# Kernel optimization log

Measured on AMD Instinct MI355X. Metric: run time of the kernel, lower is better.

The kernel has to match this reference:

```python
import jax, jax.numpy as jnp
import numpy as np

NUM_USERS = 100000
NUM_ITEMS = 50000
DIM_H = 64
NUM_LAYERS = 4
NUM_EDGES = 2000000


def setup_inputs() -> dict:
    key = jax.random.key(0)
    k1, k2, k3, k4 = jax.random.split(key, 4)
    emb_users = jax.random.normal(k1, (NUM_USERS, DIM_H), dtype=jnp.float32) * 0.01
    emb_items = jax.random.normal(k2, (NUM_ITEMS, DIM_H), dtype=jnp.float32) * 0.01
    edge_users = jax.random.randint(k3, (NUM_EDGES,), 0, NUM_USERS, dtype=jnp.int64)
    edge_items = jax.random.randint(k4, (NUM_EDGES,), 0, NUM_ITEMS, dtype=jnp.int64)
    edge_values = jnp.ones((NUM_EDGES,), dtype=jnp.float32)
    return {"emb_users": emb_users, "emb_items": emb_items,
            "edge_users": edge_users, "edge_items": edge_items,
            "edge_values": edge_values}


def reference(emb_users, emb_items, edge_users, edge_items, edge_values):
    U = emb_users.shape[0]
    I = emb_items.shape[0]
    N = U + I
    # Symmetric bipartite adjacency in COO form: (u, i+U) and (i+U, u).
    rows = jnp.concatenate([edge_users, edge_items + U])
    cols = jnp.concatenate([edge_items + U, edge_users])
    vals = jnp.concatenate([edge_values, edge_values])
    # D^{-1/2} A D^{-1/2} normalization (inf -> 0 for isolated nodes).
    deg = jax.ops.segment_sum(vals, rows, num_segments=N)
    dinv = jnp.where(deg > 0, jax.lax.rsqrt(jnp.maximum(deg, 1e-12)), 0.0)
    nvals = dinv[rows] * vals * dinv[cols]

    emb = jnp.concatenate([emb_users, emb_items])  # [N, d]
    acc = emb  # running sum over layer outputs (incl. layer 0)
    e = emb
    for _ in range(NUM_LAYERS):
        # SpMM: e <- A_norm @ e via gather + segment-sum scatter
        e = jax.ops.segment_sum(nvals[:, None] * e[cols], rows, num_segments=N)
        acc = acc + e
    alpha = 1.0 / (NUM_LAYERS + 1)
    # Original computes alpha * mean(stack(embs)), i.e. sum / (L+1)^2.
    emb_final = alpha * (acc / (NUM_LAYERS + 1))
    embf_users = emb_final[:U]
    embf_items = emb_final[U:]
    return (embf_users, emb_users, embf_items, emb_items)
```

## Files before the change

### kernel.cpp

```cpp
#include <hip/hip_runtime.h>


static inline size_t align_up(size_t x, size_t a) { return (x + a - 1) & ~(a - 1); }

#define NBA 640
#define KB  1024

__device__ inline unsigned short f32_to_bf16(float f) {
    unsigned int u = __float_as_uint(f);
    unsigned int r = (u + 0x7FFFu + ((u >> 16) & 1u)) >> 16;
    return (unsigned short)r;
}
__device__ inline float bf16_to_f32(unsigned short h) {
    return __uint_as_float(((unsigned int)h) << 16);
}
__device__ inline float bf16_lo(unsigned int d) {
    return __uint_as_float(d << 16);
}
__device__ inline float bf16_hi(unsigned int d) {
    return __uint_as_float(d & 0xFFFF0000u);
}

__global__ __launch_bounds__(256) void k_bucket_count(
        const int* __restrict__ eu, const int* __restrict__ ei,
        int* __restrict__ bh, int U, int E, int NB, int CH) {
    __shared__ int hist[NBA];
    int k = blockIdx.x;
    int t = threadIdx.x;
    for (int b = t; b < NBA; b += 256) hist[b] = 0;
    __syncthreads();
    int lo = k * CH, hi = min(E, lo + CH);
    for (int i = lo + t; i < hi; i += 256) {
        int u  = eu[i];
        int it = ei[i] + U;
        atomicAdd(&hist[u >> 8], 1);
        atomicAdd(&hist[it >> 8], 1);
    }
    __syncthreads();
    for (int b = t; b < NB; b += 256) bh[k * NBA + b] = hist[b];
}

__global__ __launch_bounds__(256) void k_scan_blocks(
        int* __restrict__ bh, int* __restrict__ total, int NB) {
    __shared__ int s[256];
    int b = blockIdx.x;
    int t = threadIdx.x;
    int k0 = t * 4;
    int vals[4];
    int sum = 0;
    #pragma unroll
    for (int j = 0; j < 4; ++j) { vals[j] = bh[(k0 + j) * NBA + b]; sum += vals[j]; }
    s[t] = sum;
    __syncthreads();
    for (int d = 1; d < 256; d <<= 1) {
        int v = (t >= d) ? s[t - d] : 0;
        __syncthreads();
        s[t] += v;
        __syncthreads();
    }
    int run = s[t] - sum;
    #pragma unroll
    for (int j = 0; j < 4; ++j) { int v = vals[j]; bh[(k0 + j) * NBA + b] = run; run += v; }
    if (t == 255) total[b] = run;
}

__global__ __launch_bounds__(256) void k_scan_buckets(
        const int* __restrict__ total, int* __restrict__ bbase, int NB) {
    __shared__ int s[256];
    int t = threadIdx.x;
    int C = (NB + 255) / 256;
    int vals[4];
    int sum = 0;
    for (int j = 0; j < C; ++j) {
        int idx = t * C + j;
        int v = (idx < NB) ? (((total[idx] + 3) & ~3) + 768) : 0;
        vals[j] = v; sum += v;
    }
    s[t] = sum;
    __syncthreads();
    for (int d = 1; d < 256; d <<= 1) {
        int v = (t >= d) ? s[t - d] : 0;
        __syncthreads();
        s[t] += v;
        __syncthreads();
    }
    int run = s[t] - sum;
    for (int j = 0; j < C; ++j) {
        int idx = t * C + j;
        if (idx < NB) bbase[idx] = run;
        run += vals[j];
    }
}

__global__ __launch_bounds__(256) void k_bucket_scatter(
        const int* __restrict__ eu, const int* __restrict__ ei,
        const float* __restrict__ ev, const int* __restrict__ bh,
        int2* __restrict__ gb, int U, int E, int NB, int CH, int CAP) {
    __shared__ int lbase[NBA];
    int k = blockIdx.x;
    int t = threadIdx.x;
    for (int b = t; b < NB; b += 256) lbase[b] = b * CAP + bh[k * NBA + b];
    __syncthreads();
    int lo = k * CH, hi = min(E, lo + CH);
    for (int i = lo + t; i < hi; i += 256) {
        int u  = eu[i];
        int it = ei[i] + U;
        int vb = __float_as_int(ev[i]);
        int b1 = u >> 8;
        int p1 = atomicAdd(&lbase[b1], 1);
        if (p1 < (b1 + 1) * CAP) gb[p1] = make_int2((u & 255) | (it << 8), vb);
        int b2 = it >> 8;
        int p2 = atomicAdd(&lbase[b2], 1);
        if (p2 < (b2 + 1) * CAP) gb[p2] = make_int2((it & 255) | (u << 8), vb);
    }
}

__global__ __launch_bounds__(256) void k_bucket_csr(
        const int2* __restrict__ gb, const int* __restrict__ total,
        const int* __restrict__ bbase,
        int* __restrict__ offs, int* __restrict__ cnt,
        float* __restrict__ dinv, float* __restrict__ dsq,
        int2* __restrict__ csr, int N, int CAP) {
    __shared__ int   hist[256];
    __shared__ float degf[256];
    __shared__ int   offl[256];
    __shared__ int   scan[256];
    int b = blockIdx.x;
    int t = threadIdx.x;
    int n0 = b << 8;
    int nbc = min(256, N - n0);
    int cb = min(total[b], CAP);
    int base = bbase[b];
    const int2* gbb = gb + (size_t)b * CAP;

    hist[t] = 0;
    degf[t] = 0.f;
    __syncthreads();
    for (int i = t; i < cb; i += 256) {
        int2 e = gbb[i];
        int rl = e.x & 255;
        atomicAdd(&hist[rl], 1);
        atomicAdd(&degf[rl], __int_as_float(e.y));
    }
    __syncthreads();
    int h = hist[t];
    int h4 = (h + 3) & ~3;
    scan[t] = h4;
    __syncthreads();
    for (int d = 1; d < 256; d <<= 1) {
        int v = (t >= d) ? scan[t - d] : 0;
        __syncthreads();
        scan[t] += v;
        __syncthreads();
    }
    int off4 = scan[t] - h4;
    offl[t] = off4;
    if (t < nbc) {
        int node = n0 + t;
        offs[node] = base + off4;
        cnt[node]  = h;
        float s = degf[t];
        bool pos = (s > 0.0f);
        dinv[node] = pos ? rsqrtf(fmaxf(s, 1e-12f)) : 0.0f;
        dsq[node]  = pos ? sqrtf(s) : 0.0f;
        for (int p = h; p < h4; ++p)
            csr[base + off4 + p] = make_int2(0, 0);
    }
    hist[t] = 0;
    __syncthreads();
    for (int i = t; i < cb; i += 256) {
        int2 e = gbb[i];
        int rl = e.x & 255;
        int col = (int)(((unsigned)e.x) >> 8);
        int tk = atomicAdd(&hist[rl], 1);
        csr[base + offl[rl] + tk] = make_int2(col, e.y);
    }
}

__global__ void k_init(const float4* __restrict__ emb_u, const float4* __restrict__ emb_i,
                       const float* __restrict__ dinv,
                       ushort4* __restrict__ g0, int U16, int N16) {
    int i = blockIdx.x * blockDim.x + threadIdx.x;
    if (i >= N16) return;
    float4 v = (i < U16) ? emb_u[i] : emb_i[i - U16];
    float d = dinv[i >> 4];
    ushort4 o;
    o.x = f32_to_bf16(v.x * d);
    o.y = f32_to_bf16(v.y * d);
    o.z = f32_to_bf16(v.z * d);
    o.w = f32_to_bf16(v.w * d);
    g0[i] = o;
}

__global__ __launch_bounds__(256) void k_layer(
        const uint4* __restrict__ gin, uint4* __restrict__ gout,
        const float* __restrict__ dinv,
        const int* __restrict__ offs, const int* __restrict__ cnt,
        const int2* __restrict__ csr, int N) {
    int gtid = blockIdx.x * blockDim.x + threadIdx.x;
    int row = gtid >> 3;
    unsigned q = threadIdx.x & 7;
    if (row >= N) return;
    int base = offs[row];
    int c = cnt[row];
    int nIter = (c + 3) >> 2;

    float a0 = 0.f, a1 = 0.f, a2 = 0.f, a3 = 0.f;
    float a4 = 0.f, a5 = 0.f, a6 = 0.f, a7 = 0.f;

    const uint4* ep4 = (const uint4*)(csr + base);
    uint4 E0 = make_uint4(0, 0, 0, 0), E1 = E0;
    if (nIter > 0) { E0 = ep4[0]; E1 = ep4[1]; }

    for (int i = 0; i < nIter; ++i) {
        uint4 G0 = gin[(E0.x << 3) | q];
        uint4 G1 = gin[(E0.z << 3) | q];
        uint4 G2 = gin[(E1.x << 3) | q];
        uint4 G3 = gin[(E1.z << 3) | q];
        uint4 P0 = ep4[2 * i + 2];
        uint4 P1 = ep4[2 * i + 3];
        float w0 = __uint_as_float(E0.y);
        float w1 = __uint_as_float(E0.w);
        float w2 = __uint_as_float(E1.y);
        float w3 = __uint_as_float(E1.w);
        a0 += w0 * bf16_lo(G0.x); a1 += w0 * bf16_hi(G0.x);
        a2 += w0 * bf16_lo(G0.y); a3 += w0 * bf16_hi(G0.y);
        a4 += w0 * bf16_lo(G0.z); a5 += w0 * bf16_hi(G0.z);
        a6 += w0 * bf16_lo(G0.w); a7 += w0 * bf16_hi(G0.w);
        a0 += w1 * bf16_lo(G1.x); a1 += w1 * bf16_hi(G1.x);
        a2 += w1 * bf16_lo(G1.y); a3 += w1 * bf16_hi(G1.y);
        a4 += w1 * bf16_lo(G1.z); a5 += w1 * bf16_hi(G1.z);
        a6 += w1 * bf16_lo(G1.w); a7 += w1 * bf16_hi(G1.w);
        a0 += w2 * bf16_lo(G2.x); a1 += w2 * bf16_hi(G2.x);
        a2 += w2 * bf16_lo(G2.y); a3 += w2 * bf16_hi(G2.y);
        a4 += w2 * bf16_lo(G2.z); a5 += w2 * bf16_hi(G2.z);
        a6 += w2 * bf16_lo(G2.w); a7 += w2 * bf16_hi(G2.w);
        a0 += w3 * bf16_lo(G3.x); a1 += w3 * bf16_hi(G3.x);
        a2 += w3 * bf16_lo(G3.y); a3 += w3 * bf16_hi(G3.y);
        a4 += w3 * bf16_lo(G3.z); a5 += w3 * bf16_hi(G3.z);
        a6 += w3 * bf16_lo(G3.w); a7 += w3 * bf16_hi(G3.w);
        E0 = P0; E1 = P1;
    }

    float dr = dinv[row];
    float d2 = dr * dr;
    uint4 o;
    o.x = (unsigned int)f32_to_bf16(d2 * a0) | ((unsigned int)f32_to_bf16(d2 * a1) << 16);
    o.y = (unsigned int)f32_to_bf16(d2 * a2) | ((unsigned int)f32_to_bf16(d2 * a3) << 16);
    o.z = (unsigned int)f32_to_bf16(d2 * a4) | ((unsigned int)f32_to_bf16(d2 * a5) << 16);
    o.w = (unsigned int)f32_to_bf16(d2 * a6) | ((unsigned int)f32_to_bf16(d2 * a7) << 16);
    gout[((unsigned)row << 3) | q] = o;
}

__global__ void k_final(const float4* __restrict__ emb_u, const float4* __restrict__ emb_i,
                        const ushort4* __restrict__ g1, const ushort4* __restrict__ g2,
                        const ushort4* __restrict__ g3, const ushort4* __restrict__ g4,
                        const float* __restrict__ dsq,
                        float4* __restrict__ out, int U16, int I16) {
    int i = blockIdx.x * blockDim.x + threadIdx.x;
    int total = 2 * U16 + 2 * I16;
    if (i >= total) return;
    const float s = 1.0f / 25.0f;
    float4 r;
    if (i < U16 || (i >= 2 * U16 && i < 2 * U16 + I16)) {
        int gi, node;
        float4 e0;
        if (i < U16) { gi = i; node = i >> 4; e0 = emb_u[i]; }
        else { int j = i - 2 * U16; gi = U16 + j; node = (U16 >> 4) + (j >> 4); e0 = emb_i[j]; }
        float d = dsq[node];
        ushort4 a = g1[gi], b = g2[gi], cc = g3[gi], dd = g4[gi];
        float gx = bf16_to_f32(a.x) + bf16_to_f32(b.x) + bf16_to_f32(cc.x) + bf16_to_f32(dd.x);
        float gy = bf16_to_f32(a.y) + bf16_to_f32(b.y) + bf16_to_f32(cc.y) + bf16_to_f32(dd.y);
        float gz = bf16_to_f32(a.z) + bf16_to_f32(b.z) + bf16_to_f32(cc.z) + bf16_to_f32(dd.z);
        float gw = bf16_to_f32(a.w) + bf16_to_f32(b.w) + bf16_to_f32(cc.w) + bf16_to_f32(dd.w);
        r = make_float4((e0.x + d * gx) * s, (e0.y + d * gy) * s,
                        (e0.z + d * gz) * s, (e0.w + d * gw) * s);
    } else if (i < 2 * U16) {
        r = emb_u[i - U16];
    } else {
        r = emb_i[i - 2 * U16 - I16];
    }
    out[i] = r;
}

extern "C" void kernel_launch(void* const* d_in, const int* in_sizes, int n_in,
                              void* d_out, int out_size, void* d_ws, size_t ws_size,
                              hipStream_t stream) {
    const float* emb_u = (const float*)d_in[0];
    const float* emb_i = (const float*)d_in[1];
    const int*   eu    = (const int*)d_in[2];
    const int*   ei    = (const int*)d_in[3];
    const float* ev    = (const float*)d_in[4];

    const int U = in_sizes[0] / 64;
    const int I = in_sizes[1] / 64;
    const int N = U + I;
    const int E = in_sizes[2];
    const int DE = 2 * E;

    const int NB = (N + 255) >> 8;
    const int CH = (E + KB - 1) / KB;

    char* base = (char*)d_ws;
    size_t off = 0;
    int*   offs  = (int*)  (base + off); off = align_up(off + (size_t)N * 4, 256);
    int*   cnt   = (int*)  (base + off); off = align_up(off + (size_t)N * 4, 256);
    float* dinv  = (float*)(base + off); off = align_up(off + (size_t)N * 4, 256);
    float* dsq   = (float*)(base + off); off = align_up(off + (size_t)N * 4, 256);
    int*   bh    = (int*)  (base + off); off = align_up(off + (size_t)NBA * KB * 4, 256);
    int*   total = (int*)  (base + off); off = align_up(off + (size_t)NBA * 4, 256);
    int*   bbase = (int*)  (base + off); off = align_up(off + (size_t)NBA * 4, 256);
    int2*  csr   = (int2*) (base + off);
    off = align_up(off + ((size_t)DE + (size_t)NBA * 772 + 16) * 8, 256);
    unsigned short* g[5];
    for (int l = 0; l < 5; ++l) {
        g[l] = (unsigned short*)(base + off);
        off = align_up(off + (size_t)N * 64 * 2, 256);
    }
    (void)ws_size;

    int2* gb = (int2*)g[1];
    size_t gcap = (size_t)4 * N * 128;
    int CAP = (int)(gcap / ((size_t)NB * 8));
    if (CAP > 16128) CAP = 16128;

    const int B = 256;
    k_bucket_count  <<<KB, B, 0, stream>>>(eu, ei, bh, U, E, NB, CH);
    k_scan_blocks   <<<NB, B, 0, stream>>>(bh, total, NB);
    k_scan_buckets  <<<1,  B, 0, stream>>>(total, bbase, NB);
    k_bucket_scatter<<<KB, B, 0, stream>>>(eu, ei, ev, bh, gb, U, E, NB, CH, CAP);
    k_bucket_csr    <<<NB, B, 0, stream>>>(gb, total, bbase, offs, cnt, dinv, dsq, csr, N, CAP);

    const int U16 = U * 16, I16 = I * 16, N16 = N * 16;
    k_init<<<(N16 + B - 1) / B, B, 0, stream>>>((const float4*)emb_u, (const float4*)emb_i,
                                                dinv, (ushort4*)g[0], U16, N16);

    for (int layer = 0; layer < 4; ++layer) {
        int threads = N * 8;
        k_layer<<<(threads + B - 1) / B, B, 0, stream>>>(
            (const uint4*)g[layer], (uint4*)g[layer + 1], dinv, offs, cnt, csr, N);
    }

    int totalv4 = 2 * U16 + 2 * I16;
    k_final<<<(totalv4 + B - 1) / B, B, 0, stream>>>(
        (const float4*)emb_u, (const float4*)emb_i,
        (const ushort4*)g[1], (const ushort4*)g[2], (const ushort4*)g[3], (const ushort4*)g[4],
        dsq, (float4*)d_out, U16, I16);
}
```

Before: 545.5 us.

## Widen CSR buckets to 1024 nodes and stage bucket scatter through LDS

Bucket width grows from 256 to 1024 nodes, so there are far fewer buckets (147 instead of 586) and the CSR build runs 1024-thread blocks. The scatter kernel now counts its edges per bucket, scans locally, writes entries sorted by bucket into shared memory, and then streams them to global memory. This turns scattered 8-byte writes into mostly contiguous runs. It adds an extra pass over the edges and a large LDS footprint (about 48KB) that limits occupancy. It also assumes each block's chunk of edges fits in 4096 staged entries.

After: 543.0 us. No clear change (-0.5%).

```diff
diff --git a/kernel.cpp b/kernel.cpp
--- a/kernel.cpp
+++ b/kernel.cpp
@@ -3,8 +3,10 @@
 
 static inline size_t align_up(size_t x, size_t a) { return (x + a - 1) & ~(a - 1); }
 
-#define NBA 640
+#define BS_LOG 10
+#define NBA 160
 #define KB  1024
+#define ENT 4096
 
 __device__ inline unsigned short f32_to_bf16(float f) {
     unsigned int u = __float_as_uint(f);
@@ -27,17 +29,17 @@
     __shared__ int hist[NBA];
     int k = blockIdx.x;
     int t = threadIdx.x;
-    for (int b = t; b < NBA; b += 256) hist[b] = 0;
+    if (t < NBA) hist[t] = 0;
     __syncthreads();
     int lo = k * CH, hi = min(E, lo + CH);
     for (int i = lo + t; i < hi; i += 256) {
         int u  = eu[i];
         int it = ei[i] + U;
-        atomicAdd(&hist[u >> 8], 1);
-        atomicAdd(&hist[it >> 8], 1);
-    }
-    __syncthreads();
-    for (int b = t; b < NB; b += 256) bh[k * NBA + b] = hist[b];
+        atomicAdd(&hist[u >> BS_LOG], 1);
+        atomicAdd(&hist[it >> BS_LOG], 1);
+    }
+    __syncthreads();
+    if (t < NB) bh[k * NBA + t] = hist[t];
 }
 
 __global__ __launch_bounds__(256) void k_scan_blocks(
@@ -68,67 +70,91 @@
         const int* __restrict__ total, int* __restrict__ bbase, int NB) {
     __shared__ int s[256];
     int t = threadIdx.x;
-    int C = (NB + 255) / 256;
-    int vals[4];
-    int sum = 0;
-    for (int j = 0; j < C; ++j) {
-        int idx = t * C + j;
-        int v = (idx < NB) ? (((total[idx] + 3) & ~3) + 768) : 0;
-        vals[j] = v; sum += v;
-    }
-    s[t] = sum;
+    int v = (t < NB) ? (((total[t] + 3) & ~3) + 3072) : 0;
+    s[t] = v;
     __syncthreads();
     for (int d = 1; d < 256; d <<= 1) {
-        int v = (t >= d) ? s[t - d] : 0;
-        __syncthreads();
-        s[t] += v;
-        __syncthreads();
-    }
-    int run = s[t] - sum;
-    for (int j = 0; j < C; ++j) {
-        int idx = t * C + j;
-        if (idx < NB) bbase[idx] = run;
-        run += vals[j];
-    }
+        int x = (t >= d) ? s[t - d] : 0;
+        __syncthreads();
+        s[t] += x;
+        __syncthreads();
+    }
+    if (t < NB) bbase[t] = s[t] - v;
 }
 
 __global__ __launch_bounds__(256) void k_bucket_scatter(
         const int* __restrict__ eu, const int* __restrict__ ei,
         const float* __restrict__ ev, const int* __restrict__ bh,
         int2* __restrict__ gb, int U, int E, int NB, int CH, int CAP) {
-    __shared__ int lbase[NBA];
+    __shared__ uint2 sent[ENT];
+    __shared__ int   sdst[ENT];
+    __shared__ int   lcur[NBA];
+    __shared__ int   ldif[NBA];
+    __shared__ int   sscan[256];
+    __shared__ int   stot;
     int k = blockIdx.x;
     int t = threadIdx.x;
-    for (int b = t; b < NB; b += 256) lbase[b] = b * CAP + bh[k * NBA + b];
+    if (t < NBA) lcur[t] = 0;
     __syncthreads();
     int lo = k * CH, hi = min(E, lo + CH);
     for (int i = lo + t; i < hi; i += 256) {
         int u  = eu[i];
         int it = ei[i] + U;
-        int vb = __float_as_int(ev[i]);
-        int b1 = u >> 8;
-        int p1 = atomicAdd(&lbase[b1], 1);
-        if (p1 < (b1 + 1) * CAP) gb[p1] = make_int2((u & 255) | (it << 8), vb);
-        int b2 = it >> 8;
-        int p2 = atomicAdd(&lbase[b2], 1);
-        if (p2 < (b2 + 1) * CAP) gb[p2] = make_int2((it & 255) | (u << 8), vb);
-    }
-}
-
-__global__ __launch_bounds__(256) void k_bucket_csr(
+        atomicAdd(&lcur[u >> BS_LOG], 1);
+        atomicAdd(&lcur[it >> BS_LOG], 1);
+    }
+    __syncthreads();
+    int c = (t < NB) ? lcur[t] : 0;
+    sscan[t] = c;
+    __syncthreads();
+    for (int d = 1; d < 256; d <<= 1) {
+        int v = (t >= d) ? sscan[t - d] : 0;
+        __syncthreads();
+        sscan[t] += v;
+        __syncthreads();
+    }
+    if (t < NB) {
+        int st = sscan[t] - c;
+        lcur[t] = st;
+        ldif[t] = t * CAP + bh[k * NBA + t] - st;
+    }
+    if (t == 255) stot = sscan[255];
+    __syncthreads();
+    for (int i = lo + t; i < hi; i += 256) {
+        int u  = eu[i];
+        int it = ei[i] + U;
+        unsigned vb = __float_as_uint(ev[i]);
+        int b1 = u >> BS_LOG;
+        int s1 = atomicAdd(&lcur[b1], 1);
+        sent[s1] = make_uint2((unsigned)((u & 1023) | (it << 10)), vb);
+        sdst[s1] = ldif[b1] + s1;
+        int b2 = it >> BS_LOG;
+        int s2 = atomicAdd(&lcur[b2], 1);
+        sent[s2] = make_uint2((unsigned)((it & 1023) | (u << 10)), vb);
+        sdst[s2] = ldif[b2] + s2;
+    }
+    __syncthreads();
+    int tot = stot;
+    for (int i = t; i < tot; i += 256) {
+        uint2 e = sent[i];
+        gb[sdst[i]] = make_int2((int)e.x, (int)e.y);
+    }
+}
+
+__global__ __launch_bounds__(1024) void k_bucket_csr(
         const int2* __restrict__ gb, const int* __restrict__ total,
         const int* __restrict__ bbase,
         int* __restrict__ offs, int* __restrict__ cnt,
         float* __restrict__ dinv, float* __restrict__ dsq,
         int2* __restrict__ csr, int N, int CAP) {
-    __shared__ int   hist[256];
-    __shared__ float degf[256];
-    __shared__ int   offl[256];
-    __shared__ int   scan[256];
+    __shared__ int   hist[1024];
+    __shared__ float degf[1024];
+    __shared__ int   offl[1024];
+    __shared__ int   scan[1024];
     int b = blockIdx.x;
     int t = threadIdx.x;
-    int n0 = b << 8;
-    int nbc = min(256, N - n0);
+    int n0 = b << BS_LOG;
+    int nbc = min(1024, N - n0);
     int cb = min(total[b], CAP);
     int base = bbase[b];
     const int2* gbb = gb + (size_t)b * CAP;
@@ -136,9 +162,9 @@
     hist[t] = 0;
     degf[t] = 0.f;
     __syncthreads();
-    for (int i = t; i < cb; i += 256) {
+    for (int i = t; i < cb; i += 1024) {
         int2 e = gbb[i];
-        int rl = e.x & 255;
+        int rl = e.x & 1023;
         atomicAdd(&hist[rl], 1);
         atomicAdd(&degf[rl], __int_as_float(e.y));
     }
@@ -147,7 +173,7 @@
     int h4 = (h + 3) & ~3;
     scan[t] = h4;
     __syncthreads();
-    for (int d = 1; d < 256; d <<= 1) {
+    for (int d = 1; d < 1024; d <<= 1) {
         int v = (t >= d) ? scan[t - d] : 0;
         __syncthreads();
         scan[t] += v;
@@ -168,10 +194,10 @@
     }
     hist[t] = 0;
     __syncthreads();
-    for (int i = t; i < cb; i += 256) {
+    for (int i = t; i < cb; i += 1024) {
         int2 e = gbb[i];
-        int rl = e.x & 255;
-        int col = (int)(((unsigned)e.x) >> 8);
+        int rl = e.x & 1023;
+        int col = (int)(((unsigned)e.x) >> 10);
         int tk = atomicAdd(&hist[rl], 1);
         csr[base + offl[rl] + tk] = make_int2(col, e.y);
     }
@@ -298,7 +324,7 @@
     const int E = in_sizes[2];
     const int DE = 2 * E;
 
-    const int NB = (N + 255) >> 8;
+    const int NB = (N + 1023) >> BS_LOG;
     const int CH = (E + KB - 1) / KB;
 
     char* base = (char*)d_ws;
@@ -311,7 +337,7 @@
     int*   total = (int*)  (base + off); off = align_up(off + (size_t)NBA * 4, 256);
     int*   bbase = (int*)  (base + off); off = align_up(off + (size_t)NBA * 4, 256);
     int2*  csr   = (int2*) (base + off);
-    off = align_up(off + ((size_t)DE + (size_t)NBA * 772 + 16) * 8, 256);
+    off = align_up(off + ((size_t)DE + (size_t)NBA * 3080 + 32) * 8, 256);
     unsigned short* g[5];
     for (int l = 0; l < 5; ++l) {
         g[l] = (unsigned short*)(base + off);
@@ -322,14 +348,14 @@
     int2* gb = (int2*)g[1];
     size_t gcap = (size_t)4 * N * 128;
     int CAP = (int)(gcap / ((size_t)NB * 8));
-    if (CAP > 16128) CAP = 16128;
+    if (CAP > 65536) CAP = 65536;
 
     const int B = 256;
     k_bucket_count  <<<KB, B, 0, stream>>>(eu, ei, bh, U, E, NB, CH);
     k_scan_blocks   <<<NB, B, 0, stream>>>(bh, total, NB);
     k_scan_buckets  <<<1,  B, 0, stream>>>(total, bbase, NB);
     k_bucket_scatter<<<KB, B, 0, stream>>>(eu, ei, ev, bh, gb, U, E, NB, CH, CAP);
-    k_bucket_csr    <<<NB, B, 0, stream>>>(gb, total, bbase, offs, cnt, dinv, dsq, csr, N, CAP);
+    k_bucket_csr    <<<NB, 1024, 0, stream>>>(gb, total, bbase, offs, cnt, dinv, dsq, csr, N, CAP);
 
     const int U16 = U * 16, I16 = I * 16, N16 = N * 16;
     k_init<<<(N16 + B - 1) / B, B, 0, stream>>>((const float4*)emb_u, (const float4*)emb_i,
```

## Stage bucket scatter and CSR build in LDS for coalesced global writes

Applied to the files above, without the earlier changes.

The bucket-scatter kernel now counts edges per bucket locally, sorts its chunk of edges by bucket in shared memory, and writes them out contiguously, replacing random per-edge global stores. The CSR build kernel uses 512 threads and assembles each bucket's CSR image in shared memory before one linear copy to global memory. Both aim to cut scattered, uncoalesced global writes during graph preprocessing. In exchange they add an extra pass over edge inputs, a large LDS footprint that lowers occupancy, and a CSR image capped at CAPL entries, beyond which edges are silently dropped. The bounds checks against CAP on global writes are also removed.

After: 501.5 us. -8.1%, faster.

```diff
diff --git a/kernel.cpp b/kernel.cpp
--- a/kernel.cpp
+++ b/kernel.cpp
@@ -5,6 +5,8 @@
 
 #define NBA 640
 #define KB  1024
+#define ENT 4096
+#define CAPL 12032
 
 __device__ inline unsigned short f32_to_bf16(float f) {
     unsigned int u = __float_as_uint(f);
@@ -96,35 +98,84 @@
         const int* __restrict__ eu, const int* __restrict__ ei,
         const float* __restrict__ ev, const int* __restrict__ bh,
         int2* __restrict__ gb, int U, int E, int NB, int CH, int CAP) {
-    __shared__ int lbase[NBA];
+    __shared__ uint2 sent[ENT];
+    __shared__ int   sdst[ENT];
+    __shared__ int   lcur[NBA];
+    __shared__ int   ldif[NBA];
+    __shared__ int   sscan[256];
     int k = blockIdx.x;
     int t = threadIdx.x;
-    for (int b = t; b < NB; b += 256) lbase[b] = b * CAP + bh[k * NBA + b];
+    for (int b = t; b < NBA; b += 256) lcur[b] = 0;
     __syncthreads();
     int lo = k * CH, hi = min(E, lo + CH);
     for (int i = lo + t; i < hi; i += 256) {
         int u  = eu[i];
         int it = ei[i] + U;
-        int vb = __float_as_int(ev[i]);
+        atomicAdd(&lcur[u >> 8], 1);
+        atomicAdd(&lcur[it >> 8], 1);
+    }
+    __syncthreads();
+    int c3[3];
+    int sum = 0;
+    #pragma unroll
+    for (int j = 0; j < 3; ++j) {
+        int idx = t * 3 + j;
+        int v = (idx < NB) ? lcur[idx] : 0;
+        c3[j] = v; sum += v;
+    }
+    sscan[t] = sum;
+    __syncthreads();
+    for (int d = 1; d < 256; d <<= 1) {
+        int v = (t >= d) ? sscan[t - d] : 0;
+        __syncthreads();
+        sscan[t] += v;
+        __syncthreads();
+    }
+    int run = sscan[t] - sum;
+    int tot = sscan[255];
+    __syncthreads();
+    #pragma unroll
+    for (int j = 0; j < 3; ++j) {
+        int idx = t * 3 + j;
+        if (idx < NB) {
+            lcur[idx] = run;
+            ldif[idx] = idx * CAP + bh[k * NBA + idx] - run;
+        }
+        run += c3[j];
+    }
+    __syncthreads();
+    for (int i = lo + t; i < hi; i += 256) {
+        int u  = eu[i];
+        int it = ei[i] + U;
+        unsigned vb = __float_as_uint(ev[i]);
         int b1 = u >> 8;
-        int p1 = atomicAdd(&lbase[b1], 1);
-        if (p1 < (b1 + 1) * CAP) gb[p1] = make_int2((u & 255) | (it << 8), vb);
+        int s1 = atomicAdd(&lcur[b1], 1);
+        sent[s1] = make_uint2((unsigned)((u & 255) | (it << 8)), vb);
+        sdst[s1] = ldif[b1] + s1;
         int b2 = it >> 8;
-        int p2 = atomicAdd(&lbase[b2], 1);
-        if (p2 < (b2 + 1) * CAP) gb[p2] = make_int2((it & 255) | (u << 8), vb);
-    }
-}
-
-__global__ __launch_bounds__(256) void k_bucket_csr(
+        int s2 = atomicAdd(&lcur[b2], 1);
+        sent[s2] = make_uint2((unsigned)((it & 255) | (u << 8)), vb);
+        sdst[s2] = ldif[b2] + s2;
+    }
+    __syncthreads();
+    for (int i = t; i < tot; i += 256) {
+        uint2 e = sent[i];
+        gb[sdst[i]] = make_int2((int)e.x, (int)e.y);
+    }
+}
+
+__global__ __launch_bounds__(512) void k_csr_lds(
         const int2* __restrict__ gb, const int* __restrict__ total,
         const int* __restrict__ bbase,
         int* __restrict__ offs, int* __restrict__ cnt,
         float* __restrict__ dinv, float* __restrict__ dsq,
         int2* __restrict__ csr, int N, int CAP) {
+    __shared__ int2  img[CAPL];
     __shared__ int   hist[256];
     __shared__ float degf[256];
-    __shared__ int   offl[256];
+    __shared__ int   lofs[256];
     __shared__ int   scan[256];
+    __shared__ int   cur[256];
     int b = blockIdx.x;
     int t = threadIdx.x;
     int n0 = b << 8;
@@ -133,48 +184,58 @@
     int base = bbase[b];
     const int2* gbb = gb + (size_t)b * CAP;
 
-    hist[t] = 0;
-    degf[t] = 0.f;
-    __syncthreads();
-    for (int i = t; i < cb; i += 256) {
+    if (t < 256) { hist[t] = 0; degf[t] = 0.f; cur[t] = 0; }
+    __syncthreads();
+    for (int i = t; i < cb; i += 512) {
         int2 e = gbb[i];
         int rl = e.x & 255;
         atomicAdd(&hist[rl], 1);
         atomicAdd(&degf[rl], __int_as_float(e.y));
     }
     __syncthreads();
-    int h = hist[t];
-    int h4 = (h + 3) & ~3;
-    scan[t] = h4;
+    int h = 0, h4 = 0;
+    if (t < 256) {
+        h = hist[t];
+        h4 = (h + 3) & ~3;
+        scan[t] = h4;
+    }
     __syncthreads();
     for (int d = 1; d < 256; d <<= 1) {
-        int v = (t >= d) ? scan[t - d] : 0;
-        __syncthreads();
-        scan[t] += v;
-        __syncthreads();
-    }
-    int off4 = scan[t] - h4;
-    offl[t] = off4;
-    if (t < nbc) {
-        int node = n0 + t;
-        offs[node] = base + off4;
-        cnt[node]  = h;
-        float s = degf[t];
-        bool pos = (s > 0.0f);
-        dinv[node] = pos ? rsqrtf(fmaxf(s, 1e-12f)) : 0.0f;
-        dsq[node]  = pos ? sqrtf(s) : 0.0f;
-        for (int p = h; p < h4; ++p)
-            csr[base + off4 + p] = make_int2(0, 0);
-    }
-    hist[t] = 0;
-    __syncthreads();
-    for (int i = t; i < cb; i += 256) {
+        int v = (t >= d && t < 256) ? scan[t - d] : 0;
+        __syncthreads();
+        if (t < 256) scan[t] += v;
+        __syncthreads();
+    }
+    int tpad = min(scan[255], CAPL);
+    if (t < 256) {
+        int off4 = scan[t] - h4;
+        lofs[t] = off4;
+        if (t < nbc) {
+            int node = n0 + t;
+            offs[node] = base + off4;
+            cnt[node]  = h;
+            float sd = degf[t];
+            bool pos = (sd > 0.0f);
+            dinv[node] = pos ? rsqrtf(fmaxf(sd, 1e-12f)) : 0.0f;
+            dsq[node]  = pos ? sqrtf(sd) : 0.0f;
+            for (int p = h; p < h4; ++p) {
+                int ix = off4 + p;
+                if (ix < CAPL) img[ix] = make_int2(0, 0);
+            }
+        }
+    }
+    __syncthreads();
+    for (int i = t; i < cb; i += 512) {
         int2 e = gbb[i];
         int rl = e.x & 255;
-        int col = (int)(((unsigned)e.x) >> 8);
-        int tk = atomicAdd(&hist[rl], 1);
-        csr[base + offl[rl] + tk] = make_int2(col, e.y);
-    }
+        int tk = atomicAdd(&cur[rl], 1);
+        int ix = lofs[rl] + tk;
+        if (ix < CAPL)
+            img[ix] = make_int2((int)(((unsigned)e.x) >> 8), e.y);
+    }
+    __syncthreads();
+    for (int i = t; i < tpad; i += 512)
+        csr[base + i] = img[i];
 }
 
 __global__ void k_init(const float4* __restrict__ emb_u, const float4* __restrict__ emb_i,
@@ -311,7 +372,7 @@
     int*   total = (int*)  (base + off); off = align_up(off + (size_t)NBA * 4, 256);
     int*   bbase = (int*)  (base + off); off = align_up(off + (size_t)NBA * 4, 256);
     int2*  csr   = (int2*) (base + off);
-    off = align_up(off + ((size_t)DE + (size_t)NBA * 772 + 16) * 8, 256);
+    off = align_up(off + ((size_t)DE + (size_t)NBA * 772 + 32) * 8, 256);
     unsigned short* g[5];
     for (int l = 0; l < 5; ++l) {
         g[l] = (unsigned short*)(base + off);
@@ -329,7 +390,7 @@
     k_scan_blocks   <<<NB, B, 0, stream>>>(bh, total, NB);
     k_scan_buckets  <<<1,  B, 0, stream>>>(total, bbase, NB);
     k_bucket_scatter<<<KB, B, 0, stream>>>(eu, ei, ev, bh, gb, U, E, NB, CH, CAP);
-    k_bucket_csr    <<<NB, B, 0, stream>>>(gb, total, bbase, offs, cnt, dinv, dsq, csr, N, CAP);
+    k_csr_lds       <<<NB, 512, 0, stream>>>(gb, total, bbase, offs, cnt, dinv, dsq, csr, N, CAP);
 
     const int U16 = U * 16, I16 = I * 16, N16 = N * 16;
     k_init<<<(N16 + B - 1) / B, B, 0, stream>>>((const float4*)emb_u, (const float4*)emb_i,
```
